# Performance work log

Measured on AMD Instinct MI355X. Metric: run time of the kernel, lower is better.

## Reference

```python
import jax, jax.numpy as jnp
import numpy as np

TOKENS, D_MODEL, VOCAB, K = 4096, 1024, 32000, 128


def setup_inputs() -> dict:
    key = jax.random.key(0)
    k1, k2 = jax.random.split(key)
    x = jax.random.normal(k1, (TOKENS, D_MODEL), dtype=jnp.float32)
    proj_weight = jax.random.normal(k2, (VOCAB, D_MODEL), dtype=jnp.float32)
    return {"x": x, "proj_weight": proj_weight, "k": K}


def reference(x, proj_weight, k):
    # faiss.knn_gpu with default METRIC_L2: squared L2 distances, k smallest.
    x_sq = jnp.sum(x * x, axis=-1, keepdims=True)            # [tokens, 1]
    b_sq = jnp.sum(proj_weight * proj_weight, axis=-1)        # [vocab]
    dots = jnp.einsum("td,vd->tv", x, proj_weight)           # [tokens, vocab]
    dist = x_sq - 2.0 * dots + b_sq[None, :]                  # [tokens, vocab]
    neg_vals, _ = jax.lax.top_k(-dist, k)                     # k smallest distances
    D = -neg_vals                                             # [tokens, k]
    return D
```

## Files before the change

### kernel.cpp

```cpp
#include <hip/hip_runtime.h>
#include <stdint.h>

#define TOKENS 4096
#define DMODEL 1024
#define VOCAB  32000
#define KSEL   128

#define BM 128
#define BN 128
#define BK 64

#define NB  2048
#define CAP 2048

typedef __attribute__((ext_vector_type(8))) short short8;
typedef __attribute__((ext_vector_type(4))) float f32x4;

__device__ __forceinline__ unsigned short f2bf(float f) {
  uint32_t u = __float_as_uint(f);
  uint32_t r = (u + 0x7fffu + ((u >> 16) & 1u)) >> 16;
  return (unsigned short)r;
}

__global__ __launch_bounds__(256)
void conv_rows(const float* __restrict__ src, unsigned short* __restrict__ dst,
               float* __restrict__ sq, int nrows) {
  int row = blockIdx.x;
  int t = threadIdx.x;
  const float4* s4 = (const float4*)(src + (size_t)row * DMODEL);
  float4 v = s4[t];
  float ss = v.x*v.x + v.y*v.y + v.z*v.z + v.w*v.w;
  uint2 pk;
  pk.x = (uint32_t)f2bf(v.x) | ((uint32_t)f2bf(v.y) << 16);
  pk.y = (uint32_t)f2bf(v.z) | ((uint32_t)f2bf(v.w) << 16);
  ((uint2*)(dst + (size_t)row * DMODEL))[t] = pk;

  __shared__ float red[256];
  red[t] = ss; __syncthreads();
  for (int s = 128; s > 0; s >>= 1) {
    if (t < s) red[t] += red[t + s];
    __syncthreads();
  }
  if (t == 0) sq[row] = red[0];
}

__global__ __launch_bounds__(256)
void gemm_dist(const unsigned short* __restrict__ Xb,
               const unsigned short* __restrict__ Wb,
               const float* __restrict__ xsq, const float* __restrict__ bsq,
               float* __restrict__ dist, int row0) {
  __shared__ unsigned short As[BM * BK];
  __shared__ unsigned short Bs[BN * BK];

  int tid  = threadIdx.x;
  int lane = tid & 63;
  int wid  = tid >> 6;
  int wr   = wid >> 1;
  int wc   = wid & 1;
  int bm   = blockIdx.y;
  int bn   = blockIdx.x;
  int rowBase = row0 + bm * BM;
  int colBase = bn * BN;

  f32x4 acc[4][4];
#pragma unroll
  for (int m = 0; m < 4; m++)
#pragma unroll
    for (int n = 0; n < 4; n++) acc[m][n] = (f32x4){0.f, 0.f, 0.f, 0.f};

  const unsigned short* Ag = Xb + (size_t)rowBase * DMODEL;
  const unsigned short* Bg = Wb + (size_t)colBase * DMODEL;

  int r16 = lane & 15;
  int kg  = lane >> 4;

  for (int kt = 0; kt < DMODEL; kt += BK) {
#pragma unroll
    for (int c = 0; c < 4; c++) {
      int g   = (c * 4 + wid) * 64 + lane;
      int r   = g >> 3;
      int col = (g & 7) * 8;
      const unsigned short* ga = Ag + (size_t)r * DMODEL + kt + col;
      const unsigned short* gb = Bg + (size_t)r * DMODEL + kt + col;
      int chunkElems = (c * 4 + wid) * 512;
      __builtin_amdgcn_global_load_lds(
          (const __attribute__((address_space(1))) void*)ga,
          (__attribute__((address_space(3))) void*)(&As[chunkElems]), 16, 0, 0);
      __builtin_amdgcn_global_load_lds(
          (const __attribute__((address_space(1))) void*)gb,
          (__attribute__((address_space(3))) void*)(&Bs[chunkElems]), 16, 0, 0);
    }
    __syncthreads();

#pragma unroll
    for (int kk = 0; kk < BK; kk += 32) {
      short8 a[4], b[4];
#pragma unroll
      for (int m = 0; m < 4; m++)
        a[m] = *(const short8*)&As[(wr * 64 + m * 16 + r16) * BK + kk + kg * 8];
#pragma unroll
      for (int n = 0; n < 4; n++)
        b[n] = *(const short8*)&Bs[(wc * 64 + n * 16 + r16) * BK + kk + kg * 8];
#pragma unroll
      for (int m = 0; m < 4; m++)
#pragma unroll
        for (int n = 0; n < 4; n++)
          acc[m][n] = __builtin_amdgcn_mfma_f32_16x16x32_bf16(a[m], b[n], acc[m][n], 0, 0, 0);
    }
    __syncthreads();
  }

  int col16 = lane & 15;
  int rg    = lane >> 4;
#pragma unroll
  for (int m = 0; m < 4; m++) {
#pragma unroll
    for (int n = 0; n < 4; n++) {
      int col = colBase + wc * 64 + n * 16 + col16;
      float bq = bsq[col];
#pragma unroll
      for (int i = 0; i < 4; i++) {
        int rowL = bm * BM + wr * 64 + m * 16 + rg * 4 + i;
        float d = xsq[row0 + rowL] + bq - 2.0f * acc[m][n][i];
        dist[(size_t)rowL * VOCAB + col] = d;
      }
    }
  }
}

__device__ __forceinline__ int binOf(float x, float mn, float invw) {
  int b = (int)((x - mn) * invw);
  return b < NB - 1 ? b : NB - 1;
}

__device__ __forceinline__ void scanFind(unsigned* bins, unsigned* s_scan,
                                         unsigned target, int* s_B,
                                         unsigned* s_cum, int t) {
  unsigned ssum = 0;
  int base = t * (NB / 256);
#pragma unroll
  for (int j = 0; j < NB / 256; j++) ssum += bins[base + j];
  s_scan[t] = ssum;
  __syncthreads();
  for (int off = 1; off < 256; off <<= 1) {
    unsigned add = (t >= off) ? s_scan[t - off] : 0u;
    __syncthreads();
    s_scan[t] += add;
    __syncthreads();
  }
  unsigned incl = s_scan[t];
  unsigned excl = incl - ssum;
  if (excl < target && incl >= target) {
    unsigned cum = excl;
    for (int j = 0; j < NB / 256; j++) {
      cum += bins[base + j];
      if (cum >= target) { *s_B = base + j; *s_cum = cum; break; }
    }
  }
  __syncthreads();
}

__global__ __launch_bounds__(256)
void select_topk(const float* __restrict__ dist, float* __restrict__ out, int row0) {
  int r = blockIdx.x;
  int t = threadIdx.x;
  const float* rowp = dist + (size_t)r * VOCAB;

  __shared__ float    s_red[256];
  __shared__ float    s_red2[256];
  __shared__ unsigned s_scan[256];
  __shared__ unsigned bins[NB];
  __shared__ float    cand[CAP];
  __shared__ unsigned s_cnt;
  __shared__ int      s_B, s_B2;
  __shared__ unsigned s_cum, s_cum2;

  float mn = 3.4e38f, mx = -3.4e38f;
  for (int i = t; i < VOCAB / 4; i += 256) {
    float4 v = ((const float4*)rowp)[i];
    mn = fminf(mn, fminf(fminf(v.x, v.y), fminf(v.z, v.w)));
    mx = fmaxf(mx, fmaxf(fmaxf(v.x, v.y), fmaxf(v.z, v.w)));
  }
  s_red[t] = mn; s_red2[t] = mx; __syncthreads();
  for (int s = 128; s > 0; s >>= 1) {
    if (t < s) {
      s_red[t]  = fminf(s_red[t],  s_red[t + s]);
      s_red2[t] = fmaxf(s_red2[t], s_red2[t + s]);
    }
    __syncthreads();
  }
  float rmn = s_red[0], rmx = s_red2[0];
  float range = rmx - rmn;

  if (!(range > 1e-20f)) {
    for (int i = t; i < KSEL; i += 256)
      out[(size_t)(row0 + r) * KSEL + i] = rmn;
    return;
  }

  float invw = (float)NB / range;

  for (int i = t; i < NB; i += 256) bins[i] = 0;
  __syncthreads();
  for (int i = t; i < VOCAB / 4; i += 256) {
    float4 v = ((const float4*)rowp)[i];
    atomicAdd(&bins[binOf(v.x, rmn, invw)], 1u);
    atomicAdd(&bins[binOf(v.y, rmn, invw)], 1u);
    atomicAdd(&bins[binOf(v.z, rmn, invw)], 1u);
    atomicAdd(&bins[binOf(v.w, rmn, invw)], 1u);
  }
  __syncthreads();

  scanFind(bins, s_scan, KSEL, &s_B, &s_cum, t);
  int B = s_B;
  unsigned cntLE = s_cum;
  unsigned below = cntLE - bins[B];
  __syncthreads();

  bool refine = (cntLE > CAP);
  float lo2 = rmn + (float)B * (range / (float)NB);
  float inv2 = invw * (float)NB;
  int B2 = 0;
  if (refine) {
    for (int i = t; i < NB; i += 256) bins[i] = 0;
    __syncthreads();
    for (int i = t; i < VOCAB; i += 256) {
      float x = rowp[i];
      if (binOf(x, rmn, invw) == B) {
        int b2 = (int)((x - lo2) * inv2);
        b2 = b2 < 0 ? 0 : (b2 > NB - 1 ? NB - 1 : b2);
        atomicAdd(&bins[b2], 1u);
      }
    }
    __syncthreads();
    scanFind(bins, s_scan, KSEL - below, &s_B2, &s_cum2, t);
    B2 = s_B2;
    __syncthreads();
  }

  if (t == 0) s_cnt = 0;
  __syncthreads();
  for (int i = t; i < VOCAB; i += 256) {
    float x = rowp[i];
    int b = binOf(x, rmn, invw);
    bool take;
    if (!refine) {
      take = (b <= B);
    } else {
      if (b < B) take = true;
      else if (b == B) {
        int b2 = (int)((x - lo2) * inv2);
        b2 = b2 < 0 ? 0 : (b2 > NB - 1 ? NB - 1 : b2);
        take = (b2 <= B2);
      } else take = false;
    }
    if (take) {
      unsigned idx = atomicAdd(&s_cnt, 1u);
      if (idx < CAP) cand[idx] = x;
    }
  }
  __syncthreads();
  int m = (int)(s_cnt < CAP ? s_cnt : CAP);

  for (int i = t; i < m; i += 256) {
    float vi = cand[i];
    int rk = 0;
    for (int j = 0; j < m; j++) {
      float vj = cand[j];
      rk += (vj < vi) || (vj == vi && j < i);
    }
    if (rk < KSEL) out[(size_t)(row0 + r) * KSEL + rk] = vi;
  }
}

extern "C" void kernel_launch(void* const* d_in, const int* in_sizes, int n_in,
                              void* d_out, int out_size, void* d_ws, size_t ws_size,
                              hipStream_t stream) {
  const float* x = (const float*)d_in[0];
  const float* w = (const float*)d_in[1];
  float* out = (float*)d_out;

  char* ws = (char*)d_ws;
  size_t off = 0;
  auto alloc = [&](size_t bytes) -> char* {
    off = (off + 255) & ~(size_t)255;
    char* p = ws + off;
    off += bytes;
    return p;
  };
  unsigned short* Xb = (unsigned short*)alloc((size_t)TOKENS * DMODEL * 2);
  unsigned short* Wb = (unsigned short*)alloc((size_t)VOCAB * DMODEL * 2);
  float* xsq = (float*)alloc((size_t)TOKENS * 4);
  float* bsq = (float*)alloc((size_t)VOCAB * 4);
  off = (off + 255) & ~(size_t)255;
  size_t fixed = off;

  int TS = TOKENS;
  while (TS > 128 && fixed + (size_t)TS * VOCAB * 4 > ws_size) TS >>= 1;
  float* dist = (float*)(ws + fixed);

  conv_rows<<<TOKENS, 256, 0, stream>>>(x, Xb, xsq, TOKENS);
  conv_rows<<<VOCAB, 256, 0, stream>>>(w, Wb, bsq, VOCAB);

  for (int row0 = 0; row0 < TOKENS; row0 += TS) {
    dim3 g(VOCAB / BN, TS / BM);
    gemm_dist<<<g, 256, 0, stream>>>(Xb, Wb, xsq, bsq, dist, row0);
    select_topk<<<TS, 256, 0, stream>>>(dist, out, row0);
  }
}
```

Before: 935.2 us.

## Store distances as bf16, fuse row min/max into GEMM epilogue, drop refine pass

The GEMM epilogue now writes distances as bf16 instead of fp32 and computes per-row min/max with shared and global atomics. This removes the separate min/max pass in the selection kernel and halves distance-buffer traffic. The selection kernel reads packed bf16 values and drops the second-level refinement histogram, and GEMM blocks are remapped with an XCD-aware grouped swizzle. Returned distances are now bf16-rounded, which may exceed tolerance. Without refinement, the candidate count can overflow CAP when a bin is dense.

```diff
diff --git a/kernel.cpp b/kernel.cpp
--- a/kernel.cpp
+++ b/kernel.cpp
@@ -20,6 +20,13 @@
   uint32_t u = __float_as_uint(f);
   uint32_t r = (u + 0x7fffu + ((u >> 16) & 1u)) >> 16;
   return (unsigned short)r;
+}
+__device__ __forceinline__ unsigned encf(float f) {
+  unsigned u = __float_as_uint(f);
+  return (u >> 31) ? ~u : (u | 0x80000000u);
+}
+__device__ __forceinline__ float decf(unsigned e) {
+  return __uint_as_float((e >> 31) ? (e & 0x7fffffffu) : ~e);
 }
 
 __global__ __launch_bounds__(256)
@@ -48,19 +55,35 @@
 void gemm_dist(const unsigned short* __restrict__ Xb,
                const unsigned short* __restrict__ Wb,
                const float* __restrict__ xsq, const float* __restrict__ bsq,
-               float* __restrict__ dist, int row0) {
+               unsigned short* __restrict__ dist,
+               unsigned* __restrict__ rminE, unsigned* __restrict__ rmaxE,
+               int row0) {
   __shared__ unsigned short As[BM * BK];
   __shared__ unsigned short Bs[BN * BK];
+  __shared__ unsigned rminS[BM], rmaxS[BM];
 
   int tid  = threadIdx.x;
   int lane = tid & 63;
   int wid  = tid >> 6;
   int wr   = wid >> 1;
   int wc   = wid & 1;
-  int bm   = blockIdx.y;
-  int bn   = blockIdx.x;
+
+  int nwg = gridDim.x * gridDim.y;
+  int bid = blockIdx.y * gridDim.x + blockIdx.x;
+  int cpx = nwg >> 3;
+  int o   = (bid & 7) * cpx + (bid >> 3);
+  int NR  = gridDim.y;
+  int GR  = (NR & 3) ? 1 : 4;
+  int span = gridDim.x * GR;
+  int sg  = o / span;
+  int rem = o - sg * span;
+  int bn  = rem / GR;
+  int bm  = sg * GR + (rem - bn * GR);
+
   int rowBase = row0 + bm * BM;
   int colBase = bn * BN;
+
+  for (int i = tid; i < BM; i += 256) { rminS[i] = 0xFFFFFFFFu; rmaxS[i] = 0u; }
 
   f32x4 acc[4][4];
 #pragma unroll
@@ -112,24 +135,41 @@
 
   int col16 = lane & 15;
   int rg    = lane >> 4;
+  float bq[4];
+#pragma unroll
+  for (int n = 0; n < 4; n++) bq[n] = bsq[colBase + wc * 64 + n * 16 + col16];
+
 #pragma unroll
   for (int m = 0; m < 4; m++) {
 #pragma unroll
-    for (int n = 0; n < 4; n++) {
-      int col = colBase + wc * 64 + n * 16 + col16;
-      float bq = bsq[col];
-#pragma unroll
-      for (int i = 0; i < 4; i++) {
-        int rowL = bm * BM + wr * 64 + m * 16 + rg * 4 + i;
-        float d = xsq[row0 + rowL] + bq - 2.0f * acc[m][n][i];
-        dist[(size_t)rowL * VOCAB + col] = d;
+    for (int i = 0; i < 4; i++) {
+      int lrow = wr * 64 + m * 16 + rg * 4 + i;
+      int rowL = bm * BM + lrow;
+      float xq = xsq[row0 + rowL];
+      float mn = 3.4e38f, mx = -3.4e38f;
+#pragma unroll
+      for (int n = 0; n < 4; n++) {
+        float d = xq + bq[n] - 2.0f * acc[m][n][i];
+        unsigned short h = f2bf(d);
+        float dr = __uint_as_float((unsigned)h << 16);
+        dist[(size_t)rowL * VOCAB + colBase + wc * 64 + n * 16 + col16] = h;
+        mn = fminf(mn, dr);
+        mx = fmaxf(mx, dr);
       }
-    }
+      atomicMin(&rminS[lrow], encf(mn));
+      atomicMax(&rmaxS[lrow], encf(mx));
+    }
+  }
+  __syncthreads();
+  if (tid < BM) {
+    atomicMin(&rminE[row0 + bm * BM + tid], rminS[tid]);
+    atomicMax(&rmaxE[row0 + bm * BM + tid], rmaxS[tid]);
   }
 }
 
 __device__ __forceinline__ int binOf(float x, float mn, float invw) {
   int b = (int)((x - mn) * invw);
+  b = b < 0 ? 0 : b;
   return b < NB - 1 ? b : NB - 1;
 }
 
@@ -161,102 +201,67 @@
 }
 
 __global__ __launch_bounds__(256)
-void select_topk(const float* __restrict__ dist, float* __restrict__ out, int row0) {
+void select_topk(const unsigned short* __restrict__ dist,
+                 const unsigned* __restrict__ rminE,
+                 const unsigned* __restrict__ rmaxE,
+                 float* __restrict__ out, int row0) {
   int r = blockIdx.x;
   int t = threadIdx.x;
-  const float* rowp = dist + (size_t)r * VOCAB;
-
-  __shared__ float    s_red[256];
-  __shared__ float    s_red2[256];
+  int grow = row0 + r;
+  const unsigned short* rowp = dist + (size_t)r * VOCAB;
+
   __shared__ unsigned s_scan[256];
   __shared__ unsigned bins[NB];
   __shared__ float    cand[CAP];
   __shared__ unsigned s_cnt;
-  __shared__ int      s_B, s_B2;
-  __shared__ unsigned s_cum, s_cum2;
-
-  float mn = 3.4e38f, mx = -3.4e38f;
-  for (int i = t; i < VOCAB / 4; i += 256) {
-    float4 v = ((const float4*)rowp)[i];
-    mn = fminf(mn, fminf(fminf(v.x, v.y), fminf(v.z, v.w)));
-    mx = fmaxf(mx, fmaxf(fmaxf(v.x, v.y), fmaxf(v.z, v.w)));
-  }
-  s_red[t] = mn; s_red2[t] = mx; __syncthreads();
-  for (int s = 128; s > 0; s >>= 1) {
-    if (t < s) {
-      s_red[t]  = fminf(s_red[t],  s_red[t + s]);
-      s_red2[t] = fmaxf(s_red2[t], s_red2[t + s]);
-    }
-    __syncthreads();
-  }
-  float rmn = s_red[0], rmx = s_red2[0];
+  __shared__ int      s_B;
+  __shared__ unsigned s_cum;
+
+  float rmn = decf(rminE[grow]);
+  float rmx = decf(rmaxE[grow]);
   float range = rmx - rmn;
 
   if (!(range > 1e-20f)) {
     for (int i = t; i < KSEL; i += 256)
-      out[(size_t)(row0 + r) * KSEL + i] = rmn;
+      out[(size_t)grow * KSEL + i] = rmn;
     return;
   }
-
   float invw = (float)NB / range;
 
   for (int i = t; i < NB; i += 256) bins[i] = 0;
   __syncthreads();
-  for (int i = t; i < VOCAB / 4; i += 256) {
-    float4 v = ((const float4*)rowp)[i];
-    atomicAdd(&bins[binOf(v.x, rmn, invw)], 1u);
-    atomicAdd(&bins[binOf(v.y, rmn, invw)], 1u);
-    atomicAdd(&bins[binOf(v.z, rmn, invw)], 1u);
-    atomicAdd(&bins[binOf(v.w, rmn, invw)], 1u);
+  const uint4* rp4 = (const uint4*)rowp;
+  for (int i = t; i < VOCAB / 8; i += 256) {
+    uint4 u = rp4[i];
+    unsigned w[4] = {u.x, u.y, u.z, u.w};
+#pragma unroll
+    for (int j = 0; j < 4; j++) {
+      float lo = __uint_as_float(w[j] << 16);
+      float hi = __uint_as_float(w[j] & 0xffff0000u);
+      atomicAdd(&bins[binOf(lo, rmn, invw)], 1u);
+      atomicAdd(&bins[binOf(hi, rmn, invw)], 1u);
+    }
   }
   __syncthreads();
 
   scanFind(bins, s_scan, KSEL, &s_B, &s_cum, t);
   int B = s_B;
-  unsigned cntLE = s_cum;
-  unsigned below = cntLE - bins[B];
-  __syncthreads();
-
-  bool refine = (cntLE > CAP);
-  float lo2 = rmn + (float)B * (range / (float)NB);
-  float inv2 = invw * (float)NB;
-  int B2 = 0;
-  if (refine) {
-    for (int i = t; i < NB; i += 256) bins[i] = 0;
-    __syncthreads();
-    for (int i = t; i < VOCAB; i += 256) {
-      float x = rowp[i];
-      if (binOf(x, rmn, invw) == B) {
-        int b2 = (int)((x - lo2) * inv2);
-        b2 = b2 < 0 ? 0 : (b2 > NB - 1 ? NB - 1 : b2);
-        atomicAdd(&bins[b2], 1u);
+
+  if (t == 0) s_cnt = 0;
+  __syncthreads();
+  for (int i = t; i < VOCAB / 8; i += 256) {
+    uint4 u = rp4[i];
+    unsigned w[4] = {u.x, u.y, u.z, u.w};
+#pragma unroll
+    for (int j = 0; j < 4; j++) {
+#pragma unroll
+      for (int h = 0; h < 2; h++) {
+        float x = __uint_as_float(h ? (w[j] & 0xffff0000u) : (w[j] << 16));
+        if (binOf(x, rmn, invw) <= B) {
+          unsigned idx = atomicAdd(&s_cnt, 1u);
+          if (idx < CAP) cand[idx] = x;
+        }
       }
-    }
-    __syncthreads();
-    scanFind(bins, s_scan, KSEL - below, &s_B2, &s_cum2, t);
-    B2 = s_B2;
-    __syncthreads();
-  }
-
-  if (t == 0) s_cnt = 0;
-  __syncthreads();
-  for (int i = t; i < VOCAB; i += 256) {
-    float x = rowp[i];
-    int b = binOf(x, rmn, invw);
-    bool take;
-    if (!refine) {
-      take = (b <= B);
-    } else {
-      if (b < B) take = true;
-      else if (b == B) {
-        int b2 = (int)((x - lo2) * inv2);
-        b2 = b2 < 0 ? 0 : (b2 > NB - 1 ? NB - 1 : b2);
-        take = (b2 <= B2);
-      } else take = false;
-    }
-    if (take) {
-      unsigned idx = atomicAdd(&s_cnt, 1u);
-      if (idx < CAP) cand[idx] = x;
     }
   }
   __syncthreads();
@@ -269,7 +274,7 @@
       float vj = cand[j];
       rk += (vj < vi) || (vj == vi && j < i);
     }
-    if (rk < KSEL) out[(size_t)(row0 + r) * KSEL + rk] = vi;
+    if (rk < KSEL) out[(size_t)grow * KSEL + rk] = vi;
   }
 }
 
@@ -292,19 +297,24 @@
   unsigned short* Wb = (unsigned short*)alloc((size_t)VOCAB * DMODEL * 2);
   float* xsq = (float*)alloc((size_t)TOKENS * 4);
   float* bsq = (float*)alloc((size_t)VOCAB * 4);
+  unsigned* rminE = (unsigned*)alloc((size_t)TOKENS * 4);
+  unsigned* rmaxE = (unsigned*)alloc((size_t)TOKENS * 4);
   off = (off + 255) & ~(size_t)255;
   size_t fixed = off;
 
   int TS = TOKENS;
-  while (TS > 128 && fixed + (size_t)TS * VOCAB * 4 > ws_size) TS >>= 1;
-  float* dist = (float*)(ws + fixed);
+  while (TS > 128 && fixed + (size_t)TS * VOCAB * 2 > ws_size) TS >>= 1;
+  unsigned short* dist = (unsigned short*)(ws + fixed);
+
+  hipMemsetAsync(rminE, 0xFF, (size_t)TOKENS * 4, stream);
+  hipMemsetAsync(rmaxE, 0x00, (size_t)TOKENS * 4, stream);
 
   conv_rows<<<TOKENS, 256, 0, stream>>>(x, Xb, xsq, TOKENS);
   conv_rows<<<VOCAB, 256, 0, stream>>>(w, Wb, bsq, VOCAB);
 
   for (int row0 = 0; row0 < TOKENS; row0 += TS) {
     dim3 g(VOCAB / BN, TS / BM);
-    gemm_dist<<<g, 256, 0, stream>>>(Xb, Wb, xsq, bsq, dist, row0);
-    select_topk<<<TS, 256, 0, stream>>>(dist, out, row0);
-  }
-}
+    gemm_dist<<<g, 256, 0, stream>>>(Xb, Wb, xsq, bsq, dist, rminE, rmaxE, row0);
+    select_topk<<<TS, 256, 0, stream>>>(dist, rminE, rmaxE, out, row0);
+  }
+}
```

Result: faster. 801.8 us (-14.3%).
